# Performance work log

Hardware: AMD Instinct MI355X
Metric: run time of the kernel (lower is better)

The kernel has to match this reference:

```python
import jax, jax.numpy as jnp
import numpy as np

D = 4096          # input_dims
P = 1             # p in Get_Atten_map_mc
NUM_IMG = 16
N_PER = 64        # objects per image
R_PER = 512       # relations per image
LN_EPS = 1e-5


def _linear_params(key, out_dim, in_dim):
    kw, kb = jax.random.split(key)
    w = jax.random.normal(kw, (out_dim, in_dim), jnp.float32) * 0.02
    b = jax.random.normal(kb, (out_dim,), jnp.float32) * 0.02
    return w, b


def setup_inputs() -> dict:
    key = jax.random.key(0)
    ks = jax.random.split(key, 12)
    N = NUM_IMG * N_PER
    R = NUM_IMG * R_PER

    obj_feats = jax.random.normal(ks[0], (N, D), jnp.float32)
    phr_feats = jax.random.normal(ks[1], (R, D), jnp.float32)

    # im_inds: uniform N_PER objects per image
    im_inds = jnp.repeat(jnp.arange(NUM_IMG, dtype=jnp.int64), N_PER)

    # rel_inds: [img_idx, subj_global, obj_global], R_PER rels per image,
    # subject/object indices local-to-image then offset to global ids.
    subj_loc = jax.random.randint(ks[2], (NUM_IMG, R_PER), 0, N_PER)
    obj_loc = jax.random.randint(ks[3], (NUM_IMG, R_PER), 0, N_PER)
    offs = (jnp.arange(NUM_IMG) * N_PER)[:, None]
    img_col = jnp.repeat(jnp.arange(NUM_IMG), R_PER)
    rel_inds = jnp.stack(
        [img_col, (subj_loc + offs).reshape(-1), (obj_loc + offs).reshape(-1)], axis=1
    ).astype(jnp.int64)

    Ws_w, Ws_b = _linear_params(ks[4], D, D)       # ws
    Wo_w, Wo_b = _linear_params(ks[5], D, D)       # wo
    Ww_w, Ww_b = _linear_params(ks[6], P, D)       # w (attention logits)
    Wc_w, Wc_b = _linear_params(ks[7], D // 2, D)  # conv Linear
    Wt1_w, Wt1_b = _linear_params(ks[8], D // 4, D)
    Wt2_w, Wt2_b = _linear_params(ks[9], D, D // 4)
    ln_g = jnp.ones((D // 4,), jnp.float32)
    ln_b = jnp.zeros((D // 4,), jnp.float32)

    return {
        "obj_feats": obj_feats, "phr_feats": phr_feats,
        "im_inds": im_inds, "rel_inds": rel_inds, "num_img": NUM_IMG,
        "Ws_w": Ws_w, "Ws_b": Ws_b, "Wo_w": Wo_w, "Wo_b": Wo_b,
        "Ww_w": Ww_w, "Ww_b": Ww_b, "Wc_w": Wc_w, "Wc_b": Wc_b,
        "Wt1_w": Wt1_w, "Wt1_b": Wt1_b, "ln_g": ln_g, "ln_b": ln_b,
        "Wt2_w": Wt2_w, "Wt2_b": Wt2_b,
    }


def reference(obj_feats, phr_feats, im_inds, rel_inds, num_img,
              Ws_w, Ws_b, Wo_w, Wo_b, Ww_w, Ww_b, Wc_w, Wc_b,
              Wt1_w, Wt1_b, ln_g, ln_b, Wt2_w, Wt2_b):
    N, d = obj_feats.shape
    n_per = N // num_img
    R = rel_inds.shape[0]
    r_per = R // num_img
    p = Ww_w.shape[0]

    # ws/wo projections over all objects (original recomputes them per image
    # on the full obj_feats -- identical math, computed once here).
    ws_all = obj_feats @ Ws_w.T + Ws_b
    wo_all = obj_feats @ Wo_w.T + Wo_b

    subj = rel_inds[:, 1]
    objc = rel_inds[:, 2]
    prod = ws_all[subj] * wo_all[objc]               # [R, D]
    atten_f = (prod * phr_feats) @ Ww_w.T + Ww_b     # [R, p]

    # conv on object features
    conv_all = jax.nn.relu(obj_feats @ Wc_w.T + Wc_b)  # [N, D/2]

    subj_i = subj.reshape(num_img, r_per)
    objc_i = objc.reshape(num_img, r_per)
    af_i = atten_f.reshape(num_img, r_per, p)
    conv_i = conv_all.reshape(num_img, n_per, -1)

    self_mask = 1.0 - jnp.eye(n_per, dtype=jnp.float32)[:, :, None]  # [n,n,1]

    def per_image(s, o, af, conv_feats):
        head = jnp.minimum(s.min(), o.min())
        A = jnp.zeros((n_per, n_per, p), jnp.float32).at[s - head, o - head].add(af)
        A = jax.nn.sigmoid(A) * self_mask
        A = A / A.sum(1)                               # [n,n,p] / [n,p] (col-normalize)
        A2 = jnp.concatenate([A, A.transpose(1, 0, 2)], axis=-1)  # [n,n,2p]
        # mc_matmul: concat of per-channel mm -> channel-major reshape
        return jnp.einsum('ijc,jd->icd', A2, conv_feats).reshape(n_per, -1)

    ctx = jax.vmap(per_image)(subj_i, objc_i, af_i, conv_i)  # [num_img, n, 2p*D/2]
    ctx = ctx.reshape(N, -1)                                  # [N, D]

    # trans: Linear -> LayerNorm -> ReLU -> Linear
    h = ctx @ Wt1_w.T + Wt1_b
    mu = h.mean(-1, keepdims=True)
    var = ((h - mu) ** 2).mean(-1, keepdims=True)
    h = (h - mu) * jax.lax.rsqrt(var + LN_EPS) * ln_g + ln_b
    h = jax.nn.relu(h)
    out = h @ Wt2_w.T + Wt2_b

    return jax.nn.relu(obj_feats + out)
```

## Files before the change

### kernel.cpp

```cpp
#include <hip/hip_runtime.h>
#include <hip/hip_bf16.h>
#include <math.h>

#define D_   4096
#define NIMG 16
#define NPER 64
#define RPER 512
#define NTOT 1024
#define RTOT 8192
#define DC   2048
#define DT   1024
#define LDW  8192

typedef __attribute__((ext_vector_type(4))) float f32x4;
typedef __attribute__((ext_vector_type(8))) short bf16x8;

#define GLD16(gp, lp) __builtin_amdgcn_global_load_lds( \
    (const __attribute__((address_space(1))) unsigned int*)(gp), \
    (__attribute__((address_space(3))) unsigned int*)(lp), 16, 0, 0)

template<int N> __device__ __forceinline__ void waitvm() {
    asm volatile("s_waitcnt vmcnt(%0)" :: "n"(N) : "memory");
}

__device__ __forceinline__ void fma4(float4& d, float s, const float4 c) {
    d.x = fmaf(s, c.x, d.x); d.y = fmaf(s, c.y, d.y);
    d.z = fmaf(s, c.z, d.z); d.w = fmaf(s, c.w, d.w);
}
__device__ __forceinline__ void st4bf(__hip_bfloat16* p, float4 v) {
    union { __hip_bfloat16 h[4]; ushort4 u; } cv;
    cv.h[0] = __float2bfloat16(v.x); cv.h[1] = __float2bfloat16(v.y);
    cv.h[2] = __float2bfloat16(v.z); cv.h[3] = __float2bfloat16(v.w);
    *(ushort4*)p = cv.u;
}
__device__ __forceinline__ float bf2f(ushort u) {
    union { float f; unsigned int i; } c; c.i = (unsigned int)u << 16; return c.f;
}
__device__ __forceinline__ ushort f2bfu(float v) {
    union { __hip_bfloat16 h; ushort u; } c; c.h = __float2bfloat16(v); return c.u;
}

__global__ __launch_bounds__(256) void cast_all(
    const float* __restrict__ obj, __hip_bfloat16* __restrict__ obj_bf,
    const float* __restrict__ Ws, const float* __restrict__ Wo,
    const float* __restrict__ Wc, __hip_bfloat16* __restrict__ wbuf,
    const float* __restrict__ Wt1, __hip_bfloat16* __restrict__ wt1r,
    const float* __restrict__ Wt2, __hip_bfloat16* __restrict__ wt2b,
    const float* __restrict__ b0, const float* __restrict__ b1,
    const float* __restrict__ b2, float* __restrict__ cb)
{
    const int b = blockIdx.x;
    const int t = threadIdx.x;
    if (b >= 26624) {
        const int i = (b - 26624) * 256 + t;
        float v;
        if (i < 4096) v = b0[i];
        else if (i < 8192) v = b1[i - 4096];
        else v = b2[i - 8192];
        cb[i] = v;
        return;
    }
    const float* s; __hip_bfloat16* d;
    if (b < 2048)       { s = obj + (size_t)b * 2048;            d = obj_bf + (size_t)b * 2048; }
    else if (b < 10240) { const int rb = b - 2048;  s = Ws + (size_t)rb * 2048; d = wbuf + (size_t)rb * 2048; }
    else if (b < 18432) { const int rb = b - 10240; s = Wo + (size_t)rb * 2048; d = wbuf + 16777216 + (size_t)rb * 2048; }
    else if (b < 22528) { const int rb = b - 18432; s = Wc + (size_t)rb * 2048; d = wbuf + 33554432 + (size_t)rb * 2048; }
    else if (b < 24576) { const int r = b - 22528;
                          s = Wt1 + (size_t)(r & 1023) * 4096 + (r >> 10) * 2048;
                          d = wt1r + (size_t)r * 2048; }
    else                { const int rb = b - 24576; s = Wt2 + (size_t)rb * 2048; d = wt2b + (size_t)rb * 2048; }
    const int i = t * 8;
    float4 v0 = *(const float4*)(s + i);
    float4 v1 = *(const float4*)(s + i + 4);
    union { __hip_bfloat16 h[8]; ushort4 u[2]; } cv;
    cv.h[0] = __float2bfloat16(v0.x); cv.h[1] = __float2bfloat16(v0.y);
    cv.h[2] = __float2bfloat16(v0.z); cv.h[3] = __float2bfloat16(v0.w);
    cv.h[4] = __float2bfloat16(v1.x); cv.h[5] = __float2bfloat16(v1.y);
    cv.h[6] = __float2bfloat16(v1.z); cv.h[7] = __float2bfloat16(v1.w);
    *(ushort4*)(d + i)     = cv.u[0];
    *(ushort4*)(d + i + 4) = cv.u[1];
}

template<int BM, int BN>
__global__ __launch_bounds__(256) void gemm_p2(
    const ushort* __restrict__ A, const ushort* __restrict__ B,
    const float* __restrict__ bias, const float* __restrict__ resid,
    float* __restrict__ C, __hip_bfloat16* __restrict__ C2,
    __hip_bfloat16* __restrict__ C3,
    int M, int K, int ldc, int mode)
{
    constexpr int MREP = BM / 32;
    constexpr int NREP = BN / 32;
    constexpr int SLOTS = (BM + BN) * 4;
    constexpr int NPW = SLOTS / 256;
    constexpr int BUFE = SLOTS * 8;

    __shared__ ushort lds[3][BUFE];

    const int t = threadIdx.x;
    const int lane = t & 63;
    const int wid = t >> 6;
    const int wr = wid >> 1, wc = wid & 1;

    const int MT = M / BM;
    const int G = gridDim.x;
    const int bid = blockIdx.x;
    const int wgid = (bid & 7) * (G >> 3) + (bid >> 3);
    const int nt = wgid / MT, mt = wgid % MT;
    const int bm = mt * BM, bn = nt * BN;

    const ushort* gp[NPW];
    int loff[NPW];
#pragma unroll
    for (int i = 0; i < NPW; ++i) {
        const int slot = i * 256 + t;
        const bool isA = slot < BM * 4;
        const int s2 = isA ? slot : slot - BM * 4;
        const int row = s2 >> 2;
        const int q = (s2 & 3) ^ ((row >> 1) & 3);
        gp[i] = (isA ? A + (size_t)(bm + row) * K : B + (size_t)(bn + row) * K) + q * 8;
        loff[i] = slot * 8;
    }

    auto stage = [&](int b, int kpos) {
#pragma unroll
        for (int i = 0; i < NPW; ++i) GLD16(gp[i] + kpos, &lds[b][loff[i]]);
    };

    int aoff[MREP], boff[NREP];
    const int sx = (((lane >> 4) ^ ((lane >> 1) & 3))) << 3;
#pragma unroll
    for (int m = 0; m < MREP; ++m)
        aoff[m] = (wr * (BM / 2) + (lane & 15) + m * 16) * 32 + sx;
#pragma unroll
    for (int n = 0; n < NREP; ++n)
        boff[n] = BM * 32 + (wc * (BN / 2) + (lane & 15) + n * 16) * 32 + sx;

    f32x4 acc[MREP][NREP] = {};

    const int NT = K >> 5;
    stage(0, 0);
    stage(1, 32);
    if constexpr (NPW == 2) waitvm<2>();
    else if constexpr (NPW == 3) waitvm<3>();
    else waitvm<4>();
    __builtin_amdgcn_sched_barrier(0);
    __builtin_amdgcn_s_barrier();
    __builtin_amdgcn_sched_barrier(0);

    for (int tt = 0; tt < NT; ++tt) {
        const bool pf = (tt + 2 < NT);
        if (pf) stage((tt + 2) % 3, (tt + 2) << 5);
        __builtin_amdgcn_sched_barrier(0);

        const ushort* lb = lds[tt % 3];
        bf16x8 af[MREP], bfv[NREP];
#pragma unroll
        for (int m = 0; m < MREP; ++m) af[m] = *(const bf16x8*)(lb + aoff[m]);
#pragma unroll
        for (int n = 0; n < NREP; ++n) bfv[n] = *(const bf16x8*)(lb + boff[n]);
#pragma unroll
        for (int m = 0; m < MREP; ++m)
#pragma unroll
            for (int n = 0; n < NREP; ++n)
                acc[m][n] = __builtin_amdgcn_mfma_f32_16x16x32_bf16(
                    af[m], bfv[n], acc[m][n], 0, 0, 0);

        __builtin_amdgcn_sched_barrier(0);
        if (pf) {
            if constexpr (NPW == 2) waitvm<2>();
            else if constexpr (NPW == 3) waitvm<3>();
            else waitvm<4>();
        } else {
            waitvm<0>();
        }
        __builtin_amdgcn_sched_barrier(0);
        __builtin_amdgcn_s_barrier();
        __builtin_amdgcn_sched_barrier(0);
    }

    const int col0 = bn + wc * (BN / 2) + (lane & 15);
    const int row0 = bm + wr * (BM / 2) + ((lane >> 4) << 2);

    if (mode == 4) {
        ushort* patch = ((ushort*)lds) + wid * (64 * 72);
        const bool doRelu = (bn >= 8192);
#pragma unroll
        for (int m = 0; m < MREP; ++m) {
#pragma unroll
            for (int n = 0; n < NREP; ++n) {
                const float bz = bias[col0 + n * 16];
#pragma unroll
                for (int rg = 0; rg < 4; ++rg) {
                    float v = acc[m][n][rg] + bz;
                    if (doRelu) v = fmaxf(v, 0.f);
                    const int lr = m * 16 + ((lane >> 4) << 2) + rg;
                    const int lc = n * 16 + (lane & 15);
                    patch[lr * 72 + lc] = f2bfu(v);
                }
            }
        }
        const int lcol8 = (lane & 7) * 8;
        const int gcol = bn + wc * (BN / 2) + lcol8;
#pragma unroll
        for (int m = 0; m < MREP; ++m) {
#pragma unroll
            for (int pass = 0; pass < 2; ++pass) {
                const int lr = m * 16 + pass * 8 + (lane >> 3);
                uint4 v4 = *(const uint4*)(patch + lr * 72 + lcol8);
                const int grow = bm + wr * (BM / 2) + lr;
                if (gcol < 8192)
                    *(uint4*)((ushort*)C2 + (size_t)grow * LDW + gcol) = v4;
                else
                    *(uint4*)((ushort*)C3 + (size_t)grow * 2048 + (gcol - 8192)) = v4;
            }
        }
        return;
    }

#pragma unroll
    for (int m = 0; m < MREP; ++m) {
#pragma unroll
        for (int n = 0; n < NREP; ++n) {
            const int cn = col0 + n * 16;
            const float bz = bias ? bias[cn] : 0.f;
#pragma unroll
            for (int rg = 0; rg < 4; ++rg) {
                const int gm = row0 + m * 16 + rg;
                float v = acc[m][n][rg] + bz;
                if (mode == 2)
                    v = fmaxf(v + resid[(size_t)gm * ldc + cn], 0.f);
                C[(size_t)gm * ldc + cn] = v;
            }
        }
    }
}

__global__ __launch_bounds__(256) void atten_kernel(
    const ushort* __restrict__ wswo, const float* __restrict__ phr,
    const int* __restrict__ rel, const float* __restrict__ Www,
    const float* __restrict__ Wwb, float* __restrict__ atten)
{
    const int r = (blockIdx.x & 7) * 1024 + (blockIdx.x >> 3);
    const int s = rel[r * 3 + 1], o = rel[r * 3 + 2];
    const int t = threadIdx.x;
    const ushort* pws = wswo + (size_t)s * LDW;
    const ushort* pwo = wswo + (size_t)o * LDW + 4096;
    const float*  pph = phr + (size_t)r * D_;
    float sum = 0.f;
#pragma unroll
    for (int half = 0; half < 2; ++half) {
        const int q = t * 8 + half * 2048;
        ushort4 w0 = *(const ushort4*)(pws + q);
        ushort4 w1 = *(const ushort4*)(pws + q + 4);
        ushort4 u0 = *(const ushort4*)(pwo + q);
        ushort4 u1 = *(const ushort4*)(pwo + q + 4);
        float4 p0 = *(const float4*)(pph + q);
        float4 p1 = *(const float4*)(pph + q + 4);
        float4 g0 = *(const float4*)(Www + q);
        float4 g1 = *(const float4*)(Www + q + 4);
        sum += bf2f(w0.x) * bf2f(u0.x) * p0.x * g0.x
             + bf2f(w0.y) * bf2f(u0.y) * p0.y * g0.y
             + bf2f(w0.z) * bf2f(u0.z) * p0.z * g0.z
             + bf2f(w0.w) * bf2f(u0.w) * p0.w * g0.w
             + bf2f(w1.x) * bf2f(u1.x) * p1.x * g1.x
             + bf2f(w1.y) * bf2f(u1.y) * p1.y * g1.y
             + bf2f(w1.z) * bf2f(u1.z) * p1.z * g1.z
             + bf2f(w1.w) * bf2f(u1.w) * p1.w * g1.w;
    }
    for (int off = 32; off > 0; off >>= 1) sum += __shfl_down(sum, off);
    __shared__ float red[4];
    if ((t & 63) == 0) red[t >> 6] = sum;
    __syncthreads();
    if (t == 0) atten[r] = red[0] + red[1] + red[2] + red[3] + Wwb[0];
}

__global__ __launch_bounds__(256) void build_A(
    const int* __restrict__ rel, const float* __restrict__ atten,
    float* __restrict__ Anorm)
{
    const int g = blockIdx.x;
    const int t = threadIdx.x;
    __shared__ float Am[64][64];
    __shared__ float S[64];
    __shared__ int headSh;
    for (int i = t; i < 4096; i += 256) ((float*)Am)[i] = 0.f;
    if (t == 0) headSh = 0x7fffffff;

    int lmin = 0x7fffffff;
    for (int rr = t; rr < RPER; rr += 256) {
        const int base = (g * RPER + rr) * 3;
        lmin = min(lmin, min(rel[base + 1], rel[base + 2]));
    }
    for (int off = 32; off > 0; off >>= 1) lmin = min(lmin, __shfl_down(lmin, off));
    __syncthreads();
    if ((t & 63) == 0) atomicMin(&headSh, lmin);
    __syncthreads();
    const int head = headSh;

    for (int rr = t; rr < RPER; rr += 256) {
        const int base = (g * RPER + rr) * 3;
        atomicAdd(&Am[rel[base + 1] - head][rel[base + 2] - head],
                  atten[g * RPER + rr]);
    }
    __syncthreads();

    for (int idx = t; idx < 4096; idx += 256) {
        const int i = idx >> 6, j = idx & 63;
        float v = 1.f / (1.f + expf(-Am[i][j]));
        if (i == j) v = 0.f;
        Am[i][j] = v;
    }
    __syncthreads();

    if (t < 64) {
        float sum = 0.f;
        for (int k = 0; k < 64; ++k) sum += Am[t][k];
        S[t] = sum;
    }
    __syncthreads();

    float* outg = Anorm + (size_t)g * 4096;
    for (int idx = t; idx < 4096; idx += 256) {
        const int j = idx & 63;
        outg[idx] = ((const float*)Am)[idx] / S[j];
    }
}

__global__ __launch_bounds__(256) void amult_ln(
    const float* __restrict__ Anorm, const float* __restrict__ P,
    const float* __restrict__ w1b, const float* __restrict__ gamma,
    const float* __restrict__ beta, __hip_bfloat16* __restrict__ hb)
{
    const int wg = (blockIdx.x & 7) * 128 + (blockIdx.x >> 3);
    const int g = wg >> 6;
    const int i = wg & 63;
    const int t = threadIdx.x;
    __shared__ float Ar[64], Ac[64];
    if (t < 64) Ar[t] = Anorm[(size_t)g * 4096 + i * 64 + t];
    else if (t < 128) { const int j = t - 64; Ac[j] = Anorm[(size_t)g * 4096 + j * 64 + i]; }
    __syncthreads();

    const float* pg = P + (size_t)g * 64 * 2048;
    float4 v = {0, 0, 0, 0};
    for (int j = 0; j < 64; ++j) {
        float4 p1 = *(const float4*)(pg + (size_t)j * 2048 + (t << 2));
        float4 p2 = *(const float4*)(pg + (size_t)j * 2048 + 1024 + (t << 2));
        fma4(v, Ar[j], p1);
        fma4(v, Ac[j], p2);
    }
    float4 b0 = *(const float4*)(w1b + (t << 2));
    v.x += b0.x; v.y += b0.y; v.z += b0.z; v.w += b0.w;

    float s  = v.x + v.y + v.z + v.w;
    float ss = v.x * v.x + v.y * v.y + v.z * v.z + v.w * v.w;
    for (int off = 32; off > 0; off >>= 1) {
        s  += __shfl_down(s, off);
        ss += __shfl_down(ss, off);
    }
    __shared__ float rs[4], rss[4];
    if ((t & 63) == 0) { rs[t >> 6] = s; rss[t >> 6] = ss; }
    __syncthreads();
    const float tot  = rs[0] + rs[1] + rs[2] + rs[3];
    const float tot2 = rss[0] + rss[1] + rss[2] + rss[3];
    const float mu   = tot * (1.f / DT);
    const float var  = tot2 * (1.f / DT) - mu * mu;
    const float rstd = rsqrtf(var + 1e-5f);
    float4 g4 = *(const float4*)(gamma + (t << 2));
    float4 b4 = *(const float4*)(beta + (t << 2));
    float4 o;
    o.x = fmaxf(fmaf((v.x - mu) * rstd, g4.x, b4.x), 0.f);
    o.y = fmaxf(fmaf((v.y - mu) * rstd, g4.y, b4.y), 0.f);
    o.z = fmaxf(fmaf((v.z - mu) * rstd, g4.z, b4.z), 0.f);
    o.w = fmaxf(fmaf((v.w - mu) * rstd, g4.w, b4.w), 0.f);
    st4bf(hb + (size_t)(g * 64 + i) * DT + (t << 2), o);
}

extern "C" void kernel_launch(void* const* d_in, const int* in_sizes, int n_in,
                              void* d_out, int out_size, void* d_ws, size_t ws_size,
                              hipStream_t stream)
{
    const float* obj   = (const float*)d_in[0];
    const float* phr   = (const float*)d_in[1];
    const int*   rel   = (const int*)d_in[3];
    const float* Ws_w  = (const float*)d_in[5];
    const float* Ws_b  = (const float*)d_in[6];
    const float* Wo_w  = (const float*)d_in[7];
    const float* Wo_b  = (const float*)d_in[8];
    const float* Ww_w  = (const float*)d_in[9];
    const float* Ww_b  = (const float*)d_in[10];
    const float* Wc_w  = (const float*)d_in[11];
    const float* Wc_b  = (const float*)d_in[12];
    const float* Wt1_w = (const float*)d_in[13];
    const float* Wt1_b = (const float*)d_in[14];
    const float* ln_g  = (const float*)d_in[15];
    const float* ln_b  = (const float*)d_in[16];
    const float* Wt2_w = (const float*)d_in[17];
    const float* Wt2_b = (const float*)d_in[18];
    float* out = (float*)d_out;

    float* ws = (float*)d_ws;
    __hip_bfloat16* wbuf    = (__hip_bfloat16*)ws;
    __hip_bfloat16* h_bf    = (__hip_bfloat16*)ws;
    __hip_bfloat16* obj_bf  = (__hip_bfloat16*)(ws + 20971520);
    float* Pbuf             = ws + 20971520;
    __hip_bfloat16* wswo_bf = (__hip_bfloat16*)(ws + 23068672);
    __hip_bfloat16* conv_bf = (__hip_bfloat16*)(ws + 27262976);
    __hip_bfloat16* wt1r    = (__hip_bfloat16*)(ws + 28311552);
    __hip_bfloat16* wt2b    = (__hip_bfloat16*)(ws + 30408704);
    float* atten  = ws + 32505856;
    float* Anorm  = ws + 32514048;
    float* cbias  = ws + 32579584;

    const dim3 blk(256);

    cast_all<<<dim3(26664), blk, 0, stream>>>(
        obj, obj_bf, Ws_w, Wo_w, Wc_w, wbuf, Wt1_w, wt1r, Wt2_w, wt2b,
        Ws_b, Wo_b, Wc_b, cbias);

    gemm_p2<128, 128><<<dim3(640), blk, 0, stream>>>(
        (const ushort*)obj_bf, (const ushort*)wbuf, cbias, nullptr,
        nullptr, wswo_bf, conv_bf, NTOT, D_, 0, 4);

    atten_kernel<<<dim3(RTOT), blk, 0, stream>>>(
        (const ushort*)wswo_bf, phr, rel, Ww_w, Ww_b, atten);
    build_A<<<dim3(NIMG), blk, 0, stream>>>(rel, atten, Anorm);

    gemm_p2<64, 64><<<dim3(512), blk, 0, stream>>>(
        (const ushort*)conv_bf, (const ushort*)wt1r, nullptr, nullptr,
        Pbuf, nullptr, nullptr, NTOT, DC, DC, 0);

    amult_ln<<<dim3(1024), blk, 0, stream>>>(Anorm, Pbuf, Wt1_b, ln_g, ln_b, h_bf);

    gemm_p2<64, 128><<<dim3(512), blk, 0, stream>>>(
        (const ushort*)h_bf, (const ushort*)wt2b, Wt2_b, obj,
        out, nullptr, nullptr, NTOT, DT, D_, 2);
}
```

Measured before the change: 289.8 us.

## Replace first fused GEMM with 256x256-tile 8-wave kernel and split-phase pipelining

The large fused Ws/Wo/Wc projection GEMM (1024x10240x4096) moves from a 128x128 tile, 4-wave kernel with 640 blocks to a dedicated 256x256 tile, 8-wave kernel with 160 blocks. Each K step is split into two halves that interleave global-to-LDS loads with MFMA bursts, and s_setprio raises priority during the matrix work. The larger tile raises arithmetic intensity and cuts redundant operand loads. The cost is that 160 blocks only partly fill the CU count, and register pressure rises with 32 accumulators per lane. The mode-4 epilogue moves out of the generic GEMM into the new kernel.

```diff
diff --git a/kernel.cpp b/kernel.cpp
--- a/kernel.cpp
+++ b/kernel.cpp
@@ -81,13 +81,145 @@
     *(ushort4*)(d + i + 4) = cv.u[1];
 }
 
+__global__ __launch_bounds__(512, 2) void gemm8v2(
+    const ushort* __restrict__ A, const ushort* __restrict__ B,
+    const float* __restrict__ bias,
+    __hip_bfloat16* __restrict__ C2, __hip_bfloat16* __restrict__ C3,
+    int M, int K)
+{
+    __shared__ ushort sh[3][16384];
+
+    const int t = threadIdx.x;
+    const int lane = t & 63;
+    const int wid = t >> 6;
+    const int wm = wid >> 2, wn = wid & 3;
+
+    const int MT = M >> 8;
+    const int G = gridDim.x;
+    const int wgid = (blockIdx.x & 7) * (G >> 3) + (blockIdx.x >> 3);
+    const int nt = wgid / MT, mt = wgid % MT;
+    const int bm = mt * 256, bn = nt * 256;
+
+    const int rA0 = t >> 2,          qA0 = (t & 3) ^ ((rA0 >> 1) & 3);
+    const int rA1 = (t + 512) >> 2,  qA1 = (t & 3) ^ ((rA1 >> 1) & 3);
+    const ushort* gA0 = A + (size_t)(bm + rA0) * K + qA0 * 8;
+    const ushort* gA1 = A + (size_t)(bm + rA1) * K + qA1 * 8;
+    const ushort* gB0 = B + (size_t)(bn + rA0) * K + qA0 * 8;
+    const ushort* gB1 = B + (size_t)(bn + rA1) * K + qA1 * 8;
+    const int dA0 = t * 8, dA1 = (t + 512) * 8;
+    const int dB0 = 8192 + t * 8, dB1 = 8192 + (t + 512) * 8;
+
+    const int sx = ((lane >> 4) ^ ((lane >> 1) & 3)) * 8;
+    int aoff[8], boff[4];
+#pragma unroll
+    for (int m = 0; m < 8; ++m)
+        aoff[m] = (wm * 128 + m * 16 + (lane & 15)) * 32 + sx;
+#pragma unroll
+    for (int n = 0; n < 4; ++n)
+        boff[n] = 8192 + (wn * 64 + n * 16 + (lane & 15)) * 32 + sx;
+
+    f32x4 acc[8][4] = {};
+    const int NT = K >> 5;
+
+    GLD16(gA0, &sh[0][dA0]); GLD16(gA1, &sh[0][dA1]);
+    GLD16(gB0, &sh[0][dB0]); GLD16(gB1, &sh[0][dB1]);
+    GLD16(gA0 + 32, &sh[1][dA0]); GLD16(gA1 + 32, &sh[1][dA1]);
+    GLD16(gB0 + 32, &sh[1][dB0]); GLD16(gB1 + 32, &sh[1][dB1]);
+    waitvm<4>();
+    __builtin_amdgcn_sched_barrier(0);
+    __builtin_amdgcn_s_barrier();
+    __builtin_amdgcn_sched_barrier(0);
+
+    for (int T = 0; T < NT; ++T) {
+        const ushort* lb = sh[T % 3];
+        ushort* nb = sh[(T + 2) % 3];
+        const bool pf = (T + 2 < NT);
+        const int kpos = (T + 2) << 5;
+
+        if (pf) { GLD16(gA0 + kpos, nb + dA0); GLD16(gA1 + kpos, nb + dA1); }
+        bf16x8 bv[4], af[4];
+#pragma unroll
+        for (int n = 0; n < 4; ++n) bv[n] = *(const bf16x8*)(lb + boff[n]);
+#pragma unroll
+        for (int m = 0; m < 4; ++m) af[m] = *(const bf16x8*)(lb + aoff[m]);
+        __builtin_amdgcn_s_barrier();
+        asm volatile("s_waitcnt lgkmcnt(0)" ::: "memory");
+        __builtin_amdgcn_sched_barrier(0);
+        __builtin_amdgcn_s_setprio(1);
+#pragma unroll
+        for (int m = 0; m < 4; ++m)
+#pragma unroll
+            for (int n = 0; n < 4; ++n)
+                acc[m][n] = __builtin_amdgcn_mfma_f32_16x16x32_bf16(
+                    af[m], bv[n], acc[m][n], 0, 0, 0);
+        __builtin_amdgcn_s_setprio(0);
+        __builtin_amdgcn_sched_barrier(0);
+        __builtin_amdgcn_s_barrier();
+
+        if (pf) { GLD16(gB0 + kpos, nb + dB0); GLD16(gB1 + kpos, nb + dB1); }
+#pragma unroll
+        for (int m = 0; m < 4; ++m) af[m] = *(const bf16x8*)(lb + aoff[4 + m]);
+        __builtin_amdgcn_s_barrier();
+        asm volatile("s_waitcnt lgkmcnt(0)" ::: "memory");
+        __builtin_amdgcn_sched_barrier(0);
+        __builtin_amdgcn_s_setprio(1);
+#pragma unroll
+        for (int m = 0; m < 4; ++m)
+#pragma unroll
+            for (int n = 0; n < 4; ++n)
+                acc[4 + m][n] = __builtin_amdgcn_mfma_f32_16x16x32_bf16(
+                    af[m], bv[n], acc[4 + m][n], 0, 0, 0);
+        __builtin_amdgcn_s_setprio(0);
+        __builtin_amdgcn_sched_barrier(0);
+        if (pf) waitvm<4>(); else waitvm<0>();
+        __builtin_amdgcn_sched_barrier(0);
+        __builtin_amdgcn_s_barrier();
+        __builtin_amdgcn_sched_barrier(0);
+    }
+
+    ushort* patch = ((ushort*)sh) + wid * (64 * 72);
+    const bool doRelu = (bn >= 8192);
+    const int lcol8 = (lane & 7) * 8;
+#pragma unroll
+    for (int chunk = 0; chunk < 2; ++chunk) {
+#pragma unroll
+        for (int m2 = 0; m2 < 4; ++m2) {
+            const int m = chunk * 4 + m2;
+#pragma unroll
+            for (int n = 0; n < 4; ++n) {
+                const float bz = bias[bn + wn * 64 + n * 16 + (lane & 15)];
+#pragma unroll
+                for (int rg = 0; rg < 4; ++rg) {
+                    float v = acc[m][n][rg] + bz;
+                    if (doRelu) v = fmaxf(v, 0.f);
+                    const int lr = m2 * 16 + ((lane >> 4) << 2) + rg;
+                    const int lc = n * 16 + (lane & 15);
+                    patch[lr * 72 + lc] = f2bfu(v);
+                }
+            }
+        }
+#pragma unroll
+        for (int m2 = 0; m2 < 4; ++m2) {
+#pragma unroll
+            for (int pass = 0; pass < 2; ++pass) {
+                const int lr = m2 * 16 + pass * 8 + (lane >> 3);
+                uint4 v4 = *(const uint4*)(patch + lr * 72 + lcol8);
+                const int grow = bm + wm * 128 + chunk * 64 + lr;
+                const int gcol = bn + wn * 64 + lcol8;
+                if (gcol < 8192)
+                    *(uint4*)((ushort*)C2 + (size_t)grow * LDW + gcol) = v4;
+                else
+                    *(uint4*)((ushort*)C3 + (size_t)grow * 2048 + (gcol - 8192)) = v4;
+            }
+        }
+    }
+}
+
 template<int BM, int BN>
 __global__ __launch_bounds__(256) void gemm_p2(
     const ushort* __restrict__ A, const ushort* __restrict__ B,
     const float* __restrict__ bias, const float* __restrict__ resid,
-    float* __restrict__ C, __hip_bfloat16* __restrict__ C2,
-    __hip_bfloat16* __restrict__ C3,
-    int M, int K, int ldc, int mode)
+    float* __restrict__ C, int M, int K, int ldc, int mode)
 {
     constexpr int MREP = BM / 32;
     constexpr int NREP = BN / 32;
@@ -181,43 +313,6 @@
 
     const int col0 = bn + wc * (BN / 2) + (lane & 15);
     const int row0 = bm + wr * (BM / 2) + ((lane >> 4) << 2);
-
-    if (mode == 4) {
-        ushort* patch = ((ushort*)lds) + wid * (64 * 72);
-        const bool doRelu = (bn >= 8192);
-#pragma unroll
-        for (int m = 0; m < MREP; ++m) {
-#pragma unroll
-            for (int n = 0; n < NREP; ++n) {
-                const float bz = bias[col0 + n * 16];
-#pragma unroll
-                for (int rg = 0; rg < 4; ++rg) {
-                    float v = acc[m][n][rg] + bz;
-                    if (doRelu) v = fmaxf(v, 0.f);
-                    const int lr = m * 16 + ((lane >> 4) << 2) + rg;
-                    const int lc = n * 16 + (lane & 15);
-                    patch[lr * 72 + lc] = f2bfu(v);
-                }
-            }
-        }
-        const int lcol8 = (lane & 7) * 8;
-        const int gcol = bn + wc * (BN / 2) + lcol8;
-#pragma unroll
-        for (int m = 0; m < MREP; ++m) {
-#pragma unroll
-            for (int pass = 0; pass < 2; ++pass) {
-                const int lr = m * 16 + pass * 8 + (lane >> 3);
-                uint4 v4 = *(const uint4*)(patch + lr * 72 + lcol8);
-                const int grow = bm + wr * (BM / 2) + lr;
-                if (gcol < 8192)
-                    *(uint4*)((ushort*)C2 + (size_t)grow * LDW + gcol) = v4;
-                else
-                    *(uint4*)((ushort*)C3 + (size_t)grow * 2048 + (gcol - 8192)) = v4;
-            }
-        }
-        return;
-    }
-
 #pragma unroll
     for (int m = 0; m < MREP; ++m) {
 #pragma unroll
@@ -418,9 +513,9 @@
         obj, obj_bf, Ws_w, Wo_w, Wc_w, wbuf, Wt1_w, wt1r, Wt2_w, wt2b,
         Ws_b, Wo_b, Wc_b, cbias);
 
-    gemm_p2<128, 128><<<dim3(640), blk, 0, stream>>>(
-        (const ushort*)obj_bf, (const ushort*)wbuf, cbias, nullptr,
-        nullptr, wswo_bf, conv_bf, NTOT, D_, 0, 4);
+    gemm8v2<<<dim3(160), dim3(512), 0, stream>>>(
+        (const ushort*)obj_bf, (const ushort*)wbuf, cbias,
+        wswo_bf, conv_bf, NTOT, D_);
 
     atten_kernel<<<dim3(RTOT), blk, 0, stream>>>(
         (const ushort*)wswo_bf, phr, rel, Ww_w, Ww_b, atten);
@@ -428,11 +523,11 @@
 
     gemm_p2<64, 64><<<dim3(512), blk, 0, stream>>>(
         (const ushort*)conv_bf, (const ushort*)wt1r, nullptr, nullptr,
-        Pbuf, nullptr, nullptr, NTOT, DC, DC, 0);
+        Pbuf, NTOT, DC, DC, 0);
 
     amult_ln<<<dim3(1024), blk, 0, stream>>>(Anorm, Pbuf, Wt1_b, ln_g, ln_b, h_bf);
 
     gemm_p2<64, 128><<<dim3(512), blk, 0, stream>>>(
         (const ushort*)h_bf, (const ushort*)wt2b, Wt2_b, obj,
-        out, nullptr, nullptr, NTOT, DT, D_, 2);
-}
+        out, NTOT, DT, D_, 2);
+}
```

Measured after the change: 288.0 us. Within noise of the previous version (-0.6%).
